# Kernel optimization log

Hardware: AMD Instinct MI355X
Metric: run time of the kernel (lower is better)

The kernel has to match this reference:

```python
import jax, jax.numpy as jnp
import numpy as np

L = 16  # block size; g = c // L; lc = c // g


def linear(x, W, b):
    # x: [..., in], W: [in, out], b: [out]
    return jnp.dot(x, W) + b


def setup_inputs() -> dict:
    key = jax.random.key(0)
    ks = jax.random.split(key, 20)
    c = 256
    L2 = L * L
    s = 0.02
    inp = {"x": jax.random.normal(ks[0], (4, 32, 32, 32, c), dtype=jnp.float32)}
    names = [("W_h", (c, c)), ("b_h", (c,)), ("W_w", (c, c)), ("b_w", (c,)),
             ("W_c", (c, c)), ("b_c", (c,)), ("W_d", (c, c)), ("b_d", (c,)),
             ("W_attn", (L2, L2)), ("b_attn", (L2,)),
             ("W_1", (c, c)), ("b_1", (c,)), ("W_2", (c, c)), ("b_2", (c,)),
             ("W_3", (c, c)), ("b_3", (c,))]
    for i, (nm, shp) in enumerate(names):
        inp[nm] = jax.random.normal(ks[i + 1], shp, dtype=jnp.float32) * s
    return inp


def ip_mlp(x, W_h, b_h, W_w, b_w, W_c, b_c, W_attn, b_attn, W_1, b_1):
    b, h, w, d, c = x.shape
    g = c // L
    lc = c // g
    h1, w1 = h // L, w // L
    # x_att: b (h1 lh) (w1 lw) d c -> b h1 w1 d c (lh lw)
    xa = x.reshape(b, h1, L, w1, L, d, c).transpose(0, 1, 3, 5, 6, 2, 4)
    xa = xa.reshape(b, h1, w1, d, c, L * L)
    xa = linear(xa, W_attn, b_attn)
    xa = xa.reshape(b, h1, w1, d, c, L, L).transpose(0, 1, 5, 2, 6, 3, 4)
    x_att = xa.reshape(b, h, w, d, c)
    # x_h: b (h1 lh) w d (lc g) -> b (h1 w) lc d (lh g)
    xh = x.reshape(b, h1, L, w, d, lc, g).transpose(0, 1, 3, 5, 4, 2, 6)
    xh = xh.reshape(b, h1 * w, lc, d, L * g)
    xh = linear(xh, W_h, b_h)
    xh = xh.reshape(b, h1, w, lc, d, L, g).transpose(0, 1, 5, 2, 4, 3, 6)
    x_h = xh.reshape(b, h, w, d, c)
    # x_w: b h (w1 lw) d (lc g) -> b (h w1) lc d (lw g)
    xw = x.reshape(b, h, w1, L, d, lc, g).transpose(0, 1, 2, 5, 4, 3, 6)
    xw = xw.reshape(b, h * w1, lc, d, L * g)
    xw = linear(xw, W_w, b_w)
    xw = xw.reshape(b, h, w1, lc, d, L, g).transpose(0, 1, 2, 5, 4, 3, 6)
    x_w = xw.reshape(b, h, w, d, c)
    x_c = linear(x, W_c, b_c)
    out = (1.0 + x_att) * (x_h + x_w + x_c)
    return linear(out, W_1, b_1)


def tp_mlp(x, W_d, b_d, W_2, b_2):
    b, h, w, d, c = x.shape
    g = c // L
    l = c // g
    d1 = d // L
    # b h w (d1 ld) (l g) -> b h w d1 l (ld g)
    xd = x.reshape(b, h, w, d1, L, l, g).transpose(0, 1, 2, 3, 5, 4, 6)
    xd = xd.reshape(b, h, w, d1, l, L * g)
    xd = linear(xd, W_d, b_d)
    xd = xd.reshape(b, h, w, d1, l, L, g).transpose(0, 1, 2, 3, 5, 4, 6)
    xd = xd.reshape(b, h, w, d, c)
    return linear(xd, W_2, b_2)


def reference(x, W_h, b_h, W_w, b_w, W_c, b_c, W_d, b_d, W_attn, b_attn,
              W_1, b_1, W_2, b_2, W_3, b_3):
    x = x + ip_mlp(x, W_h, b_h, W_w, b_w, W_c, b_c, W_attn, b_attn, W_1, b_1)
    x = x + tp_mlp(x, W_d, b_d, W_2, b_2)
    x = x + linear(x, W_3, b_3)
    return x
```

## Files before the change

kernel.cpp:

```cpp
#include <hip/hip_runtime.h>


typedef __attribute__((ext_vector_type(8))) short bf16x8;
typedef __attribute__((ext_vector_type(8))) unsigned short u16x8;
typedef __attribute__((ext_vector_type(4))) float f32x4;
typedef __attribute__((ext_vector_type(4))) unsigned short u16x4;
typedef unsigned short u16;
typedef unsigned int u32;

#define DEV __device__ __forceinline__

DEV u16 f2b(float f) {
  union { float f; u32 u; } v; v.f = f;
  u32 r = v.u + 0x7FFFu + ((v.u >> 16) & 1u);
  return (u16)(r >> 16);
}
DEV float b2f(u16 b) {
  union { u32 u; float f; } v; v.u = ((u32)b) << 16; return v.f;
}

DEV int lds_off(int row, int colByte) {
  return (row << 9) + (colByte ^ ((row & 31) << 4));
}
DEV int lds_off256(int row, int colByte) {
  return (row << 8) + (colByte ^ ((row & 15) << 4));
}
DEV bf16x8 ld_lds(const u16* lds, int row, int colByte) {
  return *(const bf16x8*)((const char*)lds + lds_off(row, colByte));
}
DEV bf16x8 ld_glb(const u16* g, int row, int kByte) {
  return *(const bf16x8*)((const char*)g + (row << 9) + kByte);
}
DEV f32x4 ldx_nt(const float* p) { return __builtin_nontemporal_load((const f32x4*)p); }
DEV void stf4_nt(float* p, f32x4 v) { __builtin_nontemporal_store(v, (f32x4*)p); }

template <int MI, int NJ>
DEV void zero_acc(f32x4 acc[MI][NJ]) {
#pragma unroll
  for (int i = 0; i < MI; ++i)
#pragma unroll
    for (int j = 0; j < NJ; ++j) {
      acc[i][j][0] = 0.f; acc[i][j][1] = 0.f; acc[i][j][2] = 0.f; acc[i][j][3] = 0.f;
    }
}

template <int MI, int NJ, typename LA, typename LB>
DEV void gemmT(LA loadA, LB loadB, f32x4 acc[MI][NJ]) {
#pragma unroll
  for (int kk = 0; kk < 8; ++kk) {
    bf16x8 a[MI], b[NJ];
#pragma unroll
    for (int i = 0; i < MI; ++i) a[i] = loadA(i, kk);
#pragma unroll
    for (int j = 0; j < NJ; ++j) b[j] = loadB(j, kk);
#pragma unroll
    for (int i = 0; i < MI; ++i)
#pragma unroll
      for (int j = 0; j < NJ; ++j)
        acc[i][j] = __builtin_amdgcn_mfma_f32_16x16x32_bf16(a[i], b[j], acc[i][j], 0, 0, 0);
  }
}

#define WAVE_SETUP                  \
  const int tid = threadIdx.x;      \
  const int lane = tid & 63;        \
  const int wave = tid >> 6;        \
  const int wm = wave >> 2;         \
  const int wn = wave & 3;          \
  const int lr = lane & 15;         \
  const int lk = lane >> 4;

__global__ void k_pack_all(const float* W0, const float* W1p, const float* W2p,
                           const float* W3p, const float* W4p, const float* W5p,
                           const float* W6p, const float* W7p, u16* __restrict__ WT) {
  int bi = blockIdx.x;
  int wsel = bi >> 8, n = bi & 255;
  const float* W;
  switch (wsel) {
    case 0: W = W0; break; case 1: W = W1p; break; case 2: W = W2p; break;
    case 3: W = W3p; break; case 4: W = W4p; break; case 5: W = W5p; break;
    case 6: W = W6p; break; default: W = W7p; break;
  }
  u16* dst = WT + wsel * 65536;
  int k0 = threadIdx.x * 4;
#pragma unroll
  for (int i = 0; i < 4; ++i) {
    int k = k0 + i;
    float v = __builtin_nontemporal_load(W + k * 256 + n);
    if (wsel == 7 && k == n) v += 1.0f;
    dst[n * 256 + k] = f2b(v);
  }
}

__global__ __launch_bounds__(512, 4) void k_att(const float* __restrict__ x,
    const u16* __restrict__ WTattn, const float* __restrict__ b_attn,
    u16* __restrict__ att, u16* __restrict__ xbf) {
  __shared__ alignas(16) u16 XT[32768];
  WAVE_SETUP;
  const int ch = blockIdx.x & 1;
  const int t = blockIdx.x >> 1;
  const int d = t & 31, w1 = (t >> 5) & 1, h1 = (t >> 6) & 1, b = t >> 7;
  const int B0 = (((b * 32 + h1 * 16) * 32 + w1 * 16) * 32 + d) * 256;

  for (int i = tid; i < 8192; i += 512) {
    int q = i >> 5;
    int c4 = (i & 31) << 2;
    const int gofs = B0 + (q >> 4) * 262144 + (q & 15) * 8192 + ch * 128 + c4;
    const f32x4 v = ldx_nt(x + gofs);
    u16x4 pk;
    pk[0] = f2b(v[0]); pk[1] = f2b(v[1]); pk[2] = f2b(v[2]); pk[3] = f2b(v[3]);
    XT[lds_off(c4 + 0, q * 2) >> 1] = pk[0];
    XT[lds_off(c4 + 1, q * 2) >> 1] = pk[1];
    XT[lds_off(c4 + 2, q * 2) >> 1] = pk[2];
    XT[lds_off(c4 + 3, q * 2) >> 1] = pk[3];
    *(u16x4*)(xbf + gofs) = pk;
  }
  __syncthreads();

  f32x4 acc[8][2];
  zero_acc<8, 2>(acc);
  gemmT<8, 2>(
      [&](int i, int kk) { return ld_glb(WTattn, wm * 128 + i * 16 + lr, kk * 64 + lk * 16); },
      [&](int j, int kk) { return ld_lds(XT, wn * 32 + j * 16 + lr, kk * 64 + lk * 16); },
      acc);

  __syncthreads();
#pragma unroll
  for (int i = 0; i < 8; ++i)
#pragma unroll
    for (int j = 0; j < 2; ++j)
#pragma unroll
      for (int r = 0; r < 4; ++r) {
        int p = wm * 128 + i * 16 + lk * 4 + r;
        int cl = wn * 32 + j * 16 + lr;
        XT[lds_off256(p, cl * 2) >> 1] = f2b(acc[i][j][r] + b_attn[p]);
      }
  __syncthreads();
  u16* out = att + t * 65536;
  for (int i = tid; i < 4096; i += 512) {
    int p = i >> 4, sB = (i & 15) << 4;
    bf16x8 v = *(const bf16x8*)((const char*)XT + p * 256 + sB);
    int c8l = (sB ^ ((p & 15) << 4)) >> 1;
    *(bf16x8*)(out + p * 256 + ch * 128 + c8l) = v;
  }
}

__global__ __launch_bounds__(512, 1) void k_hw(const u16* __restrict__ xbf,
    const u16* __restrict__ WTh, const u16* __restrict__ WTw,
    u16* __restrict__ h_out, u16* __restrict__ w_out) {
  __shared__ alignas(16) u16 XS[65536];
  __shared__ alignas(16) u16 BB[16384];
  WAVE_SETUP;
  const int t = blockIdx.x;
  const int d = t & 31, w1 = (t >> 5) & 1, h1 = (t >> 6) & 1, b = t >> 7;
  const int B0 = (((b * 32 + h1 * 16) * 32 + w1 * 16) * 32 + d) * 256;
  u16* h_t = h_out + t * 65536;
  u16* w_t = w_out + t * 65536;

  for (int i = tid; i < 8192; i += 512) {
    int pos = i >> 5, c8 = (i & 31) << 3;
    u16x8 v = *(const u16x8*)(xbf + B0 + (pos >> 4) * 262144 + (pos & 15) * 8192 + c8);
    *(u16x8*)((char*)XS + lds_off(pos, c8 * 2)) = v;
  }
  __syncthreads();

  for (int s = 0; s < 4; ++s) {
    f32x4 hacc[8][1];
    zero_acc<8, 1>(hacc);
    gemmT<8, 1>(
        [&](int i, int kk) {
          int k = kk * 32 + lk * 8;
          return *(const bf16x8*)((const char*)XS +
                                  lds_off((k >> 4) * 16 + lr, (wm * 8 + i) * 32 + (k & 15) * 2));
        },
        [&](int j, int kk) { return ld_glb(WTh, s * 64 + wn * 16 + lr, kk * 64 + lk * 16); },
        hacc);
    __syncthreads();
#pragma unroll
    for (int i = 0; i < 8; ++i)
#pragma unroll
      for (int r = 0; r < 4; ++r)
        BB[lds_off(wn * 16 + lk * 4 + r, ((wm * 8 + i) * 16 + lr) * 2) >> 1] = f2b(hacc[i][0][r]);
    __syncthreads();
    for (int i2 = tid; i2 < 2048; i2 += 512) {
      int posl = i2 >> 5, sB = (i2 & 31) << 4;
      bf16x8 v = *(const bf16x8*)((const char*)BB + posl * 512 + sB);
      int c8 = (sB ^ ((posl & 31) << 4)) >> 1;
      *(bf16x8*)(h_t + (s * 64 + posl) * 256 + c8) = v;
    }
  }

  for (int q = 0; q < 4; ++q) {
    f32x4 wacc[8][1];
    zero_acc<8, 1>(wacc);
    gemmT<8, 1>(
        [&](int i, int kk) {
          int k = kk * 32 + lk * 8;
          return *(const bf16x8*)((const char*)XS +
                                  lds_off(lr * 16 + (k >> 4), (wm * 8 + i) * 32 + (k & 15) * 2));
        },
        [&](int j, int kk) { return ld_glb(WTw, q * 64 + wn * 16 + lr, kk * 64 + lk * 16); },
        wacc);
    __syncthreads();
#pragma unroll
    for (int i = 0; i < 8; ++i)
#pragma unroll
      for (int r = 0; r < 4; ++r)
        BB[lds_off((lk * 4 + r) * 4 + wn, ((wm * 8 + i) * 16 + lr) * 2) >> 1] = f2b(wacc[i][0][r]);
    __syncthreads();
    for (int i2 = tid; i2 < 2048; i2 += 512) {
      int rb = i2 >> 5, sB = (i2 & 31) << 4;
      bf16x8 v = *(const bf16x8*)((const char*)BB + rb * 512 + sB);
      int c8 = (sB ^ ((rb & 31) << 4)) >> 1;
      int pos = (rb >> 2) * 16 + 4 * q + (rb & 3);
      *(bf16x8*)(w_t + pos * 256 + c8) = v;
    }
  }
}

__global__ __launch_bounds__(512, 2) void k_comb(const u16* __restrict__ xbf,
    const u16* __restrict__ h_out, const u16* __restrict__ w_out, const u16* __restrict__ att,
    const float* __restrict__ bh, const float* __restrict__ bw, const float* __restrict__ bc,
    const u16* __restrict__ WTc, const u16* __restrict__ WT1, const float* __restrict__ b1,
    u16* __restrict__ x1) {
  __shared__ alignas(16) u16 T[32768];
  WAVE_SETUP;
  const int ph = blockIdx.x & 1;
  const int t = blockIdx.x >> 1;
  const int d = t & 31, w1 = (t >> 5) & 1, h1 = (t >> 6) & 1, b = t >> 7;
  const int B0 = (((b * 32 + h1 * 16) * 32 + w1 * 16) * 32 + d) * 256;
  const u16* h_t = h_out + t * 65536;
  const u16* w_t = w_out + t * 65536;
  const u16* att_t = att + t * 65536;

  for (int i = tid; i < 4096; i += 512) {
    int posl = i >> 5, c8 = (i & 31) << 3;
    int pos = ph * 128 + posl;
    u16x8 v = *(const u16x8*)(xbf + B0 + (pos >> 4) * 262144 + (pos & 15) * 8192 + c8);
    *(u16x8*)((char*)T + lds_off(posl, c8 * 2)) = v;
  }
  __syncthreads();

  f32x4 acc[4][4];
  zero_acc<4, 4>(acc);
  gemmT<4, 4>(
      [&](int i, int kk) { return ld_lds(T, wm * 64 + i * 16 + lr, kk * 64 + lk * 16); },
      [&](int j, int kk) { return ld_glb(WTc, wn * 64 + j * 16 + lr, kk * 64 + lk * 16); },
      acc);
  __syncthreads();

#pragma unroll
  for (int i = 0; i < 4; ++i) {
    int lh = ph * 8 + wm * 4 + i;
#pragma unroll
    for (int j = 0; j < 4; ++j) {
      float bcv = bc[wn * 64 + j * 16 + lr];
#pragma unroll
      for (int r = 0; r < 4; ++r) {
        int posl = wm * 64 + i * 16 + lk * 4 + r;
        int n = wn * 64 + j * 16 + lr;
        float v = acc[i][j][r] + bcv + bh[lh * 16 + lr] + bw[(lk * 4 + r) * 16 + lr];
        T[lds_off(posl, n * 2) >> 1] = f2b(v);
      }
    }
  }
  __syncthreads();

  for (int i2 = tid; i2 < 4096; i2 += 512) {
    int posl = i2 >> 5, c8 = (i2 & 31) << 3;
    int pos = ph * 128 + posl;
    u16x8 hv = *(const u16x8*)(h_t + pos * 256 + c8);
    u16x8 wv = *(const u16x8*)(w_t + pos * 256 + c8);
    u16x8 av = *(const u16x8*)(att_t + pos * 256 + c8);
    u16x8* p = (u16x8*)((char*)T + lds_off(posl, c8 * 2));
    u16x8 cur = *p, o;
#pragma unroll
    for (int j = 0; j < 8; ++j)
      o[j] = f2b((1.0f + b2f(av[j])) * (b2f(cur[j]) + b2f(hv[j]) + b2f(wv[j])));
    *p = o;
  }
  __syncthreads();

  zero_acc<4, 4>(acc);
  gemmT<4, 4>(
      [&](int i, int kk) { return ld_lds(T, wm * 64 + i * 16 + lr, kk * 64 + lk * 16); },
      [&](int j, int kk) { return ld_glb(WT1, wn * 64 + j * 16 + lr, kk * 64 + lk * 16); },
      acc);
  __syncthreads();

#pragma unroll
  for (int i = 0; i < 4; ++i)
#pragma unroll
    for (int j = 0; j < 4; ++j) {
      float b1v = b1[wn * 64 + j * 16 + lr];
#pragma unroll
      for (int r = 0; r < 4; ++r) {
        int posl = wm * 64 + i * 16 + lk * 4 + r;
        int n = wn * 64 + j * 16 + lr;
        T[lds_off(posl, n * 2) >> 1] = f2b(acc[i][j][r] + b1v);
      }
    }
  __syncthreads();

  for (int i2 = tid; i2 < 4096; i2 += 512) {
    int posl = i2 >> 5, sB = (i2 & 31) << 4;
    bf16x8 v = *(const bf16x8*)((const char*)T + posl * 512 + sB);
    int c8 = (sB ^ ((posl & 31) << 4)) >> 1;
    int pos = ph * 128 + posl;
    const int gofs = B0 + (pos >> 4) * 262144 + (pos & 15) * 8192 + c8;
    u16x8 xv = *(const u16x8*)(xbf + gofs);
    u16x8 o;
#pragma unroll
    for (int j = 0; j < 8; ++j) o[j] = f2b(b2f((u16)v[j]) + b2f(xv[j]));
    *(u16x8*)(x1 + gofs) = o;
  }
}

__global__ __launch_bounds__(512, 2) void k_tp(const u16* __restrict__ x1,
    const u16* __restrict__ WTd, const u16* __restrict__ WT2, const u16* __restrict__ WT3p,
    const float* __restrict__ bd, const float* __restrict__ b2, const float* __restrict__ b3,
    float* __restrict__ outp) {
  __shared__ alignas(16) u16 XS[16384];
  __shared__ alignas(16) u16 BB[16384];
  WAVE_SETUP;
  const int bid = blockIdx.x;
  const int wg = bid & 7, d1 = (bid >> 3) & 1, h = (bid >> 4) & 31, b = bid >> 9;
  const int W0 = (b * 32 + h) * 32 + wg * 4;

  for (int i = tid; i < 2048; i += 512) {
    int Rl = i >> 5, c8 = (i & 31) << 3;
    const u16x8 v = *(const u16x8*)(x1 + (size_t)(W0 + (Rl >> 4)) * 8192 +
                                    (d1 * 16 + (Rl & 15)) * 256 + c8);
    *(u16x8*)((char*)XS + lds_off(Rl, c8 * 2)) = v;
  }
  __syncthreads();

  f32x4 acc[2][4];
  zero_acc<2, 4>(acc);
  gemmT<2, 4>(
      [&](int i, int kk) {
        int k = kk * 32 + lk * 8;
        int mt = wm * 2 + i;
        return *(const bf16x8*)((const char*)XS + lds_off(mt * 16 + (k >> 4),
                                                          lr * 32 + (k & 15) * 2));
      },
      [&](int j, int kk) { return ld_glb(WTd, wn * 64 + j * 16 + lr, kk * 64 + lk * 16); },
      acc);
#pragma unroll
  for (int i = 0; i < 2; ++i)
#pragma unroll
    for (int j = 0; j < 4; ++j)
#pragma unroll
      for (int r = 0; r < 4; ++r) {
        int mloc = wm * 32 + i * 16 + lk * 4 + r;
        int n = wn * 64 + j * 16 + lr;
        int row = ((mloc >> 4) << 4) + (n >> 4);
        int col = ((mloc & 15) << 4) + (n & 15);
        BB[lds_off(row, col * 2) >> 1] = f2b(acc[i][j][r] + bd[n]);
      }
  __syncthreads();

  zero_acc<2, 4>(acc);
  gemmT<2, 4>(
      [&](int i, int kk) { return ld_lds(BB, (wm * 2 + i) * 16 + lr, kk * 64 + lk * 16); },
      [&](int j, int kk) { return ld_glb(WT2, wn * 64 + j * 16 + lr, kk * 64 + lk * 16); },
      acc);
  __syncthreads();

#pragma unroll
  for (int i = 0; i < 2; ++i)
#pragma unroll
    for (int j = 0; j < 4; ++j) {
      float b2v = b2[wn * 64 + j * 16 + lr];
#pragma unroll
      for (int r = 0; r < 4; ++r) {
        int mloc = wm * 32 + i * 16 + lk * 4 + r;
        int n = wn * 64 + j * 16 + lr;
        int off = lds_off(mloc, n * 2) >> 1;
        BB[off] = f2b(b2f(XS[off]) + acc[i][j][r] + b2v);
      }
    }
  __syncthreads();

  zero_acc<2, 4>(acc);
  gemmT<2, 4>(
      [&](int i, int kk) { return ld_lds(BB, (wm * 2 + i) * 16 + lr, kk * 64 + lk * 16); },
      [&](int j, int kk) { return ld_glb(WT3p, wn * 64 + j * 16 + lr, kk * 64 + lk * 16); },
      acc);

  float* XSf = (float*)XS;
#pragma unroll
  for (int half = 0; half < 2; ++half) {
    __syncthreads();
    if (wm == half) {
#pragma unroll
      for (int i = 0; i < 2; ++i)
#pragma unroll
        for (int j = 0; j < 4; ++j)
#pragma unroll
          for (int r = 0; r < 4; ++r) {
            int row = i * 16 + lk * 4 + r;
            int n = wn * 64 + j * 16 + lr;
            XSf[row * 256 + n] = acc[i][j][r] + b3[n];
          }
    }
    __syncthreads();
    for (int i2 = tid; i2 < 2048; i2 += 512) {
      int row = i2 >> 6, c4 = (i2 & 63) << 2;
      int Rg = half * 32 + row;
      f32x4 v = *(const f32x4*)(XSf + row * 256 + c4);
      stf4_nt(outp + (size_t)(W0 + (Rg >> 4)) * 8192 + (d1 * 16 + (Rg & 15)) * 256 + c4, v);
    }
  }
}

extern "C" void kernel_launch(void* const* d_in, const int* in_sizes, int n_in,
                              void* d_out, int out_size, void* d_ws, size_t ws_size,
                              hipStream_t stream) {
  (void)in_sizes; (void)n_in; (void)out_size; (void)ws_size;
  const float* x      = (const float*)d_in[0];
  const float* W_h    = (const float*)d_in[1];
  const float* b_h    = (const float*)d_in[2];
  const float* W_w    = (const float*)d_in[3];
  const float* b_w    = (const float*)d_in[4];
  const float* W_c    = (const float*)d_in[5];
  const float* b_c    = (const float*)d_in[6];
  const float* W_d    = (const float*)d_in[7];
  const float* b_d    = (const float*)d_in[8];
  const float* W_attn = (const float*)d_in[9];
  const float* b_attn = (const float*)d_in[10];
  const float* W_1    = (const float*)d_in[11];
  const float* b_1    = (const float*)d_in[12];
  const float* W_2    = (const float*)d_in[13];
  const float* b_2    = (const float*)d_in[14];
  const float* W_3    = (const float*)d_in[15];
  const float* b_3    = (const float*)d_in[16];
  float* outp = (float*)d_out;

  u16* WT = (u16*)d_ws;
  u16* R1 = WT + 8 * 65536;
  u16* R2 = R1 + 33554432;
  u16* HOS = (u16*)d_out;
  u16* WOS = HOS + 33554432;

  k_pack_all<<<2048, 64, 0, stream>>>(W_h, W_w, W_c, W_attn, W_1, W_d, W_2, W_3, WT);

  k_att <<<1024, 512, 0, stream>>>(x, WT + 3 * 65536, b_attn, R2, R1);
  k_hw  <<<512, 512, 0, stream>>>(R1, WT + 0 * 65536, WT + 1 * 65536, HOS, WOS);
  k_comb<<<1024, 512, 0, stream>>>(R1, HOS, WOS, R2, b_h, b_w, b_c,
                                   WT + 2 * 65536, WT + 4 * 65536, b_1, R1);
  k_tp  <<<2048, 512, 0, stream>>>(R1, WT + 5 * 65536, WT + 6 * 65536, WT + 7 * 65536,
                                   b_d, b_2, b_3, outp);
}
```

Measured before the change: 552.0 us.

## Widen k_hw to 1024 threads and shrink k_tp LDS to a single buffer

```diff
diff --git a/kernel.cpp b/kernel.cpp
--- a/kernel.cpp
+++ b/kernel.cpp
@@ -145,19 +145,23 @@
   }
 }
 
-__global__ __launch_bounds__(512, 1) void k_hw(const u16* __restrict__ xbf,
+__global__ __launch_bounds__(1024, 4) void k_hw(const u16* __restrict__ xbf,
     const u16* __restrict__ WTh, const u16* __restrict__ WTw,
     u16* __restrict__ h_out, u16* __restrict__ w_out) {
   __shared__ alignas(16) u16 XS[65536];
   __shared__ alignas(16) u16 BB[16384];
-  WAVE_SETUP;
+  const int tid = threadIdx.x;
+  const int lane = tid & 63;
+  const int wv = tid >> 6;
+  const int lr = lane & 15;
+  const int lk = lane >> 4;
   const int t = blockIdx.x;
   const int d = t & 31, w1 = (t >> 5) & 1, h1 = (t >> 6) & 1, b = t >> 7;
   const int B0 = (((b * 32 + h1 * 16) * 32 + w1 * 16) * 32 + d) * 256;
   u16* h_t = h_out + t * 65536;
   u16* w_t = w_out + t * 65536;
 
-  for (int i = tid; i < 8192; i += 512) {
+  for (int i = tid; i < 8192; i += 1024) {
     int pos = i >> 5, c8 = (i & 31) << 3;
     u16x8 v = *(const u16x8*)(xbf + B0 + (pos >> 4) * 262144 + (pos & 15) * 8192 + c8);
     *(u16x8*)((char*)XS + lds_off(pos, c8 * 2)) = v;
@@ -165,24 +169,24 @@
   __syncthreads();
 
   for (int s = 0; s < 4; ++s) {
-    f32x4 hacc[8][1];
-    zero_acc<8, 1>(hacc);
-    gemmT<8, 1>(
+    f32x4 hacc[1][4];
+    zero_acc<1, 4>(hacc);
+    gemmT<1, 4>(
         [&](int i, int kk) {
           int k = kk * 32 + lk * 8;
           return *(const bf16x8*)((const char*)XS +
-                                  lds_off((k >> 4) * 16 + lr, (wm * 8 + i) * 32 + (k & 15) * 2));
+                                  lds_off((k >> 4) * 16 + lr, wv * 32 + (k & 15) * 2));
         },
-        [&](int j, int kk) { return ld_glb(WTh, s * 64 + wn * 16 + lr, kk * 64 + lk * 16); },
+        [&](int j, int kk) { return ld_glb(WTh, s * 64 + j * 16 + lr, kk * 64 + lk * 16); },
         hacc);
     __syncthreads();
 #pragma unroll
-    for (int i = 0; i < 8; ++i)
+    for (int j = 0; j < 4; ++j)
 #pragma unroll
       for (int r = 0; r < 4; ++r)
-        BB[lds_off(wn * 16 + lk * 4 + r, ((wm * 8 + i) * 16 + lr) * 2) >> 1] = f2b(hacc[i][0][r]);
-    __syncthreads();
-    for (int i2 = tid; i2 < 2048; i2 += 512) {
+        BB[lds_off(j * 16 + lk * 4 + r, (wv * 16 + lr) * 2) >> 1] = f2b(hacc[0][j][r]);
+    __syncthreads();
+    for (int i2 = tid; i2 < 2048; i2 += 1024) {
       int posl = i2 >> 5, sB = (i2 & 31) << 4;
       bf16x8 v = *(const bf16x8*)((const char*)BB + posl * 512 + sB);
       int c8 = (sB ^ ((posl & 31) << 4)) >> 1;
@@ -191,24 +195,24 @@
   }
 
   for (int q = 0; q < 4; ++q) {
-    f32x4 wacc[8][1];
-    zero_acc<8, 1>(wacc);
-    gemmT<8, 1>(
+    f32x4 wacc[1][4];
+    zero_acc<1, 4>(wacc);
+    gemmT<1, 4>(
         [&](int i, int kk) {
           int k = kk * 32 + lk * 8;
           return *(const bf16x8*)((const char*)XS +
-                                  lds_off(lr * 16 + (k >> 4), (wm * 8 + i) * 32 + (k & 15) * 2));
+                                  lds_off(lr * 16 + (k >> 4), wv * 32 + (k & 15) * 2));
         },
-        [&](int j, int kk) { return ld_glb(WTw, q * 64 + wn * 16 + lr, kk * 64 + lk * 16); },
+        [&](int j, int kk) { return ld_glb(WTw, q * 64 + j * 16 + lr, kk * 64 + lk * 16); },
         wacc);
     __syncthreads();
 #pragma unroll
-    for (int i = 0; i < 8; ++i)
+    for (int j = 0; j < 4; ++j)
 #pragma unroll
       for (int r = 0; r < 4; ++r)
-        BB[lds_off((lk * 4 + r) * 4 + wn, ((wm * 8 + i) * 16 + lr) * 2) >> 1] = f2b(wacc[i][0][r]);
-    __syncthreads();
-    for (int i2 = tid; i2 < 2048; i2 += 512) {
+        BB[lds_off((lk * 4 + r) * 4 + j, (wv * 16 + lr) * 2) >> 1] = f2b(wacc[0][j][r]);
+    __syncthreads();
+    for (int i2 = tid; i2 < 2048; i2 += 1024) {
       int rb = i2 >> 5, sB = (i2 & 31) << 4;
       bf16x8 v = *(const bf16x8*)((const char*)BB + rb * 512 + sB);
       int c8 = (sB ^ ((rb & 31) << 4)) >> 1;
@@ -316,12 +320,11 @@
   }
 }
 
-__global__ __launch_bounds__(512, 2) void k_tp(const u16* __restrict__ x1,
+__global__ __launch_bounds__(512, 4) void k_tp(const u16* __restrict__ x1,
     const u16* __restrict__ WTd, const u16* __restrict__ WT2, const u16* __restrict__ WT3p,
     const float* __restrict__ bd, const float* __restrict__ b2, const float* __restrict__ b3,
     float* __restrict__ outp) {
-  __shared__ alignas(16) u16 XS[16384];
-  __shared__ alignas(16) u16 BB[16384];
+  __shared__ alignas(16) u16 T[16384];
   WAVE_SETUP;
   const int bid = blockIdx.x;
   const int wg = bid & 7, d1 = (bid >> 3) & 1, h = (bid >> 4) & 31, b = bid >> 9;
@@ -331,7 +334,7 @@
     int Rl = i >> 5, c8 = (i & 31) << 3;
     const u16x8 v = *(const u16x8*)(x1 + (size_t)(W0 + (Rl >> 4)) * 8192 +
                                     (d1 * 16 + (Rl & 15)) * 256 + c8);
-    *(u16x8*)((char*)XS + lds_off(Rl, c8 * 2)) = v;
+    *(u16x8*)((char*)T + lds_off(Rl, c8 * 2)) = v;
   }
   __syncthreads();
 
@@ -341,11 +344,13 @@
       [&](int i, int kk) {
         int k = kk * 32 + lk * 8;
         int mt = wm * 2 + i;
-        return *(const bf16x8*)((const char*)XS + lds_off(mt * 16 + (k >> 4),
-                                                          lr * 32 + (k & 15) * 2));
+        return *(const bf16x8*)((const char*)T + lds_off(mt * 16 + (k >> 4),
+                                                         lr * 32 + (k & 15) * 2));
       },
       [&](int j, int kk) { return ld_glb(WTd, wn * 64 + j * 16 + lr, kk * 64 + lk * 16); },
       acc);
+  __syncthreads();
+
 #pragma unroll
   for (int i = 0; i < 2; ++i)
 #pragma unroll
@@ -356,13 +361,13 @@
         int n = wn * 64 + j * 16 + lr;
         int row = ((mloc >> 4) << 4) + (n >> 4);
         int col = ((mloc & 15) << 4) + (n & 15);
-        BB[lds_off(row, col * 2) >> 1] = f2b(acc[i][j][r] + bd[n]);
+        T[lds_off(row, col * 2) >> 1] = f2b(acc[i][j][r] + bd[n]);
       }
   __syncthreads();
 
   zero_acc<2, 4>(acc);
   gemmT<2, 4>(
-      [&](int i, int kk) { return ld_lds(BB, (wm * 2 + i) * 16 + lr, kk * 64 + lk * 16); },
+      [&](int i, int kk) { return ld_lds(T, (wm * 2 + i) * 16 + lr, kk * 64 + lk * 16); },
       [&](int j, int kk) { return ld_glb(WT2, wn * 64 + j * 16 + lr, kk * 64 + lk * 16); },
       acc);
   __syncthreads();
@@ -376,19 +381,30 @@
       for (int r = 0; r < 4; ++r) {
         int mloc = wm * 32 + i * 16 + lk * 4 + r;
         int n = wn * 64 + j * 16 + lr;
-        int off = lds_off(mloc, n * 2) >> 1;
-        BB[off] = f2b(b2f(XS[off]) + acc[i][j][r] + b2v);
+        T[lds_off(mloc, n * 2) >> 1] = f2b(acc[i][j][r] + b2v);
       }
     }
+  __syncthreads();
+
+  for (int i = tid; i < 2048; i += 512) {
+    int Rl = i >> 5, c8 = (i & 31) << 3;
+    const u16x8 xv = *(const u16x8*)(x1 + (size_t)(W0 + (Rl >> 4)) * 8192 +
+                                     (d1 * 16 + (Rl & 15)) * 256 + c8);
+    u16x8* p = (u16x8*)((char*)T + lds_off(Rl, c8 * 2));
+    u16x8 cur = *p, o;
+#pragma unroll
+    for (int j = 0; j < 8; ++j) o[j] = f2b(b2f(cur[j]) + b2f(xv[j]));
+    *p = o;
+  }
   __syncthreads();
 
   zero_acc<2, 4>(acc);
   gemmT<2, 4>(
-      [&](int i, int kk) { return ld_lds(BB, (wm * 2 + i) * 16 + lr, kk * 64 + lk * 16); },
+      [&](int i, int kk) { return ld_lds(T, (wm * 2 + i) * 16 + lr, kk * 64 + lk * 16); },
       [&](int j, int kk) { return ld_glb(WT3p, wn * 64 + j * 16 + lr, kk * 64 + lk * 16); },
       acc);
 
-  float* XSf = (float*)XS;
+  float* Tf = (float*)T;
 #pragma unroll
   for (int half = 0; half < 2; ++half) {
     __syncthreads();
@@ -401,14 +417,14 @@
           for (int r = 0; r < 4; ++r) {
             int row = i * 16 + lk * 4 + r;
             int n = wn * 64 + j * 16 + lr;
-            XSf[row * 256 + n] = acc[i][j][r] + b3[n];
+            Tf[row * 256 + n] = acc[i][j][r] + b3[n];
           }
     }
     __syncthreads();
     for (int i2 = tid; i2 < 2048; i2 += 512) {
       int row = i2 >> 6, c4 = (i2 & 63) << 2;
       int Rg = half * 32 + row;
-      f32x4 v = *(const f32x4*)(XSf + row * 256 + c4);
+      f32x4 v = *(const f32x4*)(Tf + row * 256 + c4);
       stf4_nt(outp + (size_t)(W0 + (Rg >> 4)) * 8192 + (d1 * 16 + (Rg & 15)) * 256 + c4, v);
     }
   }
@@ -446,7 +462,7 @@
   k_pack_all<<<2048, 64, 0, stream>>>(W_h, W_w, W_c, W_attn, W_1, W_d, W_2, W_3, WT);
 
   k_att <<<1024, 512, 0, stream>>>(x, WT + 3 * 65536, b_attn, R2, R1);
-  k_hw  <<<512, 512, 0, stream>>>(R1, WT + 0 * 65536, WT + 1 * 65536, HOS, WOS);
+  k_hw  <<<512, 1024, 0, stream>>>(R1, WT + 0 * 65536, WT + 1 * 65536, HOS, WOS);
   k_comb<<<1024, 512, 0, stream>>>(R1, HOS, WOS, R2, b_h, b_w, b_c,
                                    WT + 2 * 65536, WT + 4 * 65536, b_1, R1);
   k_tp  <<<2048, 512, 0, stream>>>(R1, WT + 5 * 65536, WT + 6 * 65536, WT + 7 * 65536,
```

After: 703.3 us. 1.27x slower.
